# Kernel optimization log

Measured on AMD Instinct MI355X. Metric: run time of the kernel, lower is better.

Reference implementation:

```python
import jax, jax.numpy as jnp
import numpy as np

B, S = 4, 4096          # batch, tokens (64x64 SAM ViT-H grid)
DIN, DOUT = 1280, 3840  # qkv linear dims
RANK = 16
NUM_SHARED = 1
NUM_ROUTED = 6
TOP_K = 3


def setup_inputs() -> dict:
    key = jax.random.key(0)
    ks = jax.random.split(key, 9)
    s = 0.02
    return {
        "x": jax.random.normal(ks[0], (B, S, DIN), dtype=jnp.float32),
        "base_w": jax.random.normal(ks[1], (DIN, DOUT), dtype=jnp.float32) * s,
        "base_b": jax.random.normal(ks[2], (DOUT,), dtype=jnp.float32) * s,
        "shared_w1": jax.random.normal(ks[3], (NUM_SHARED, DIN, RANK), dtype=jnp.float32) * s,
        "shared_w2": jax.random.normal(ks[4], (NUM_SHARED, RANK, DOUT), dtype=jnp.float32) * s,
        "routed_w1": jax.random.normal(ks[5], (NUM_ROUTED, DIN, RANK), dtype=jnp.float32) * s,
        "routed_w2": jax.random.normal(ks[6], (NUM_ROUTED, RANK, DOUT), dtype=jnp.float32) * s,
        "router_w": jax.random.normal(ks[7], (DIN, NUM_ROUTED), dtype=jnp.float32) * s,
        "router_b": jax.random.normal(ks[8], (NUM_ROUTED,), dtype=jnp.float32) * s,
    }


def reference(x, base_w, base_b, shared_w1, shared_w2, routed_w1, routed_w2, router_w, router_b):
    b, s, din = x.shape
    # base linear runs under torch.no_grad() -> stop_gradient
    base = jax.lax.stop_gradient(jnp.einsum('bsi,io->bso', x, base_w) + base_b)
    # shared low-rank experts, summed over the shared set
    shared = jnp.einsum('bsi,eir,ero->bso', x, shared_w1, shared_w2)
    # router: softmax gates, top-k selection
    gates = jax.nn.softmax(x @ router_w + router_b, axis=-1)      # [B,S,E]
    topk_w, topk_idx = jax.lax.top_k(gates, TOP_K)                # [B,S,K]
    T = b * s
    xf = x.reshape(T, din)
    # combine weights: per-token weight for each expert (top-k indices are
    # distinct, so scatter-add reproduces the per-slot assignment exactly)
    cw = jnp.zeros((T, NUM_ROUTED), dtype=x.dtype).at[
        jnp.arange(T)[:, None], topk_idx.reshape(T, TOP_K)
    ].add(topk_w.reshape(T, TOP_K))                               # [T,E]
    # routed experts: contract rank and expert dims without materializing [T,E,DOUT]
    h = jnp.einsum('ti,eir->ter', xf, routed_w1)                  # [T,E,RANK]
    routed = jnp.einsum('ter,ero,te->to', h, routed_w2, cw).reshape(b, s, DOUT)
    return base + shared + routed
```

## Files before the change

kernel.cpp:

```cpp
#include <hip/hip_runtime.h>
#include <cstdint>
#include <cstddef>

#define DIN 1280
#define DOUT 3840
#define NEXP 6
#define RANK 16
#define TOKENS 16384
#define KPAD 1408
#define NLOW 128

typedef __bf16 bf16x8 __attribute__((ext_vector_type(8)));
typedef float f32x4 __attribute__((ext_vector_type(4)));
typedef unsigned short u16x8 __attribute__((ext_vector_type(8)));

__device__ __forceinline__ unsigned short f2bf(float f) {
    unsigned u = __builtin_bit_cast(unsigned, f);
    u += 0x7fff + ((u >> 16) & 1);
    return (unsigned short)(u >> 16);
}

__device__ __forceinline__ void async_load16(void* lds, const void* g) {
    __builtin_amdgcn_global_load_lds(
        (const __attribute__((address_space(1))) unsigned int*)g,
        (__attribute__((address_space(3))) unsigned int*)lds, 16, 0, 0);
}

__global__ void prep_w2t(const float* __restrict__ base_w,
                         const float* __restrict__ shared_w2,
                         const float* __restrict__ routed_w2,
                         unsigned short* __restrict__ WT) {
    __shared__ unsigned short tile[32][33];
    int k0 = blockIdx.x * 32, n0 = blockIdx.y * 32;
    int tx = threadIdx.x, ty = threadIdx.y;
#pragma unroll
    for (int j = 0; j < 4; j++) {
        int k = k0 + ty + j * 8;
        int n = n0 + tx;
        float v;
        if (k < DIN)            v = base_w[(size_t)k * DOUT + n];
        else if (k < DIN + 16)  v = shared_w2[(size_t)(k - DIN) * DOUT + n];
        else if (k < DIN + 112) v = routed_w2[(size_t)(k - DIN - 16) * DOUT + n];
        else                    v = 0.f;
        tile[ty + j * 8][tx] = f2bf(v);
    }
    __syncthreads();
#pragma unroll
    for (int j = 0; j < 4; j++) {
        int n = n0 + ty + j * 8;
        int k = k0 + tx;
        WT[(size_t)n * KPAD + k] = tile[tx][ty + j * 8];
    }
}

__global__ void prep_w1t(const float* __restrict__ shared_w1,
                         const float* __restrict__ routed_w1,
                         unsigned short* __restrict__ W1T) {
    __shared__ unsigned short tile[32][33];
    int k0 = blockIdx.x * 32, n0 = blockIdx.y * 32;
    int tx = threadIdx.x, ty = threadIdx.y;
#pragma unroll
    for (int j = 0; j < 4; j++) {
        int k = k0 + ty + j * 8;
        int n = n0 + tx;
        float v = 0.f;
        if (n < 16) v = shared_w1[k * RANK + n];
        else if (n < 112) {
            int jj = n - 16, e = jj >> 4, r = jj & 15;
            v = routed_w1[(size_t)e * DIN * RANK + k * RANK + r];
        }
        tile[ty + j * 8][tx] = f2bf(v);
    }
    __syncthreads();
#pragma unroll
    for (int j = 0; j < 4; j++) {
        int n = n0 + ty + j * 8;
        int k = k0 + tx;
        W1T[(size_t)n * DIN + k] = tile[tx][ty + j * 8];
    }
}

__global__ __launch_bounds__(256) void router_kernel(
    const float* __restrict__ x,
    const float* __restrict__ router_w,
    const float* __restrict__ router_b,
    unsigned short* __restrict__ A,
    float* __restrict__ cw) {
    int tid = threadIdx.x;
    size_t t0 = (size_t)blockIdx.x * 8;
    const float* xblk = x + t0 * DIN;
    unsigned short* Ablk = A + t0 * KPAD;

    for (int i = tid; i < 8 * (DIN / 8); i += 256) {
        int t = i / (DIN / 8), c = (i - t * (DIN / 8)) * 8;
        const float* xs = xblk + (size_t)t * DIN + c;
        f32x4 v0 = *(const f32x4*)xs;
        f32x4 v1 = *(const f32x4*)(xs + 4);
        u16x8 o;
#pragma unroll
        for (int j = 0; j < 4; j++) { o[j] = f2bf(v0[j]); o[4 + j] = f2bf(v1[j]); }
        *(u16x8*)&Ablk[(size_t)t * KPAD + c] = o;
    }
    if (tid < 128) {
        int t = tid >> 4, c = tid & 15;
        Ablk[t * KPAD + DIN + 112 + c] = 0;
    }

    int tg = tid >> 5, lj = tid & 31;
    const float* xt = xblk + (size_t)tg * DIN;
    float acc[6] = {0.f, 0.f, 0.f, 0.f, 0.f, 0.f};
    for (int k = lj; k < DIN; k += 32) {
        float xv = xt[k];
        const float* wr = router_w + k * NEXP;
#pragma unroll
        for (int e = 0; e < NEXP; e++) acc[e] = fmaf(xv, wr[e], acc[e]);
    }
#pragma unroll
    for (int off = 16; off > 0; off >>= 1)
#pragma unroll
        for (int e = 0; e < NEXP; e++) acc[e] += __shfl_xor(acc[e], off);

    float mx = -1e30f;
#pragma unroll
    for (int e = 0; e < NEXP; e++) { acc[e] += router_b[e]; mx = fmaxf(mx, acc[e]); }
    float g[6]; float s = 0.f;
#pragma unroll
    for (int e = 0; e < NEXP; e++) { g[e] = __expf(acc[e] - mx); s += g[e]; }
    float inv = 1.f / s;
    if (lj < NEXP) {
        float ge = g[lj];
        int cnt = 0;
#pragma unroll
        for (int e = 0; e < NEXP; e++) {
            if (e == lj) continue;
            if (g[e] > ge || (g[e] == ge && e < lj)) cnt++;
        }
        cw[(t0 + tg) * NEXP + lj] = (cnt < 3) ? ge * inv : 0.f;
    }
}

__global__ __launch_bounds__(256) void combine_kernel(
    const float* __restrict__ H, const float* __restrict__ cw,
    unsigned short* __restrict__ A) {
    int i = blockIdx.x * 256 + threadIdx.x;
    int t = i / 112, j = i - t * 112;
    float h = H[(size_t)t * NLOW + j] + H[(size_t)TOKENS * NLOW + (size_t)t * NLOW + j];
    float f = (j < 16) ? 1.0f : cw[t * NEXP + ((j - 16) >> 4)];
    A[(size_t)t * KPAD + DIN + j] = f2bf(f * h);
}

__global__ __launch_bounds__(256, 2) void gemm_small(
    const unsigned short* __restrict__ A,
    const unsigned short* __restrict__ BT,
    float* __restrict__ H) {
    __shared__ unsigned short ldsA[128 * 32];
    __shared__ unsigned short ldsB[128 * 32];
    const int KS = DIN / 2;
    int tid = threadIdx.x;
    int lane = tid & 63, wave = tid >> 6;
    int m0 = blockIdx.y * 128;
    int z = blockIdx.z;
    int wm = (wave >> 1) * 64, wn = (wave & 1) * 64;
    int lr = lane & 15, quad = lane >> 4;

    f32x4 acc[4][4] = {};
    const unsigned short* Abase = A + (size_t)m0 * KPAD + z * KS;
    const unsigned short* Bbase = BT + z * KS;
    float* Cbase = H + (size_t)z * TOKENS * NLOW;

    for (int k0 = 0; k0 < KS; k0 += 32) {
#pragma unroll
        for (int i = 0; i < 2; i++) {
            int c = i * 256 + tid;
            int row = c >> 2;
            int col = (c & 3) << 3;
            async_load16(&ldsA[(i * 256 + wave * 64) * 8],
                         Abase + (size_t)row * KPAD + k0 + col);
            async_load16(&ldsB[(i * 256 + wave * 64) * 8],
                         Bbase + (size_t)row * DIN + k0 + col);
        }
        __syncthreads();
        bf16x8 af[4], bf[4];
#pragma unroll
        for (int mi = 0; mi < 4; mi++)
            af[mi] = *(const bf16x8*)&ldsA[(wm + mi * 16 + lr) * 32 + quad * 8];
#pragma unroll
        for (int ni = 0; ni < 4; ni++)
            bf[ni] = *(const bf16x8*)&ldsB[(wn + ni * 16 + lr) * 32 + quad * 8];
#pragma unroll
        for (int mi = 0; mi < 4; mi++)
#pragma unroll
            for (int ni = 0; ni < 4; ni++)
                acc[mi][ni] = __builtin_amdgcn_mfma_f32_16x16x32_bf16(
                    af[mi], bf[ni], acc[mi][ni], 0, 0, 0);
        __syncthreads();
    }
#pragma unroll
    for (int ni = 0; ni < 4; ni++) {
        int gn = wn + ni * 16 + lr;
#pragma unroll
        for (int mi = 0; mi < 4; mi++) {
            int gm = m0 + wm + mi * 16 + quad * 4;
            f32x4 v = acc[mi][ni];
#pragma unroll
            for (int r = 0; r < 4; r++)
                Cbase[(size_t)(gm + r) * NLOW + gn] = v[r];
        }
    }
}


#define BM 256
#define BN 128
#define BKS 32

__global__ __launch_bounds__(512, 4) void gemm256(
    const unsigned short* __restrict__ A,
    const unsigned short* __restrict__ BT,
    const float* __restrict__ bias,
    float* __restrict__ C) {
    __shared__ unsigned short lA[2][BM * BKS];
    __shared__ unsigned short lB[2][BN * BKS];

    int tid = threadIdx.x;
    int lane = tid & 63, wave = tid >> 6;
    int bid = blockIdx.x;
    int xcd = bid & 7, lid = bid >> 3;
    int mt = xcd * 8 + (lid & 7);
    int nt = lid >> 3;
    int m0 = mt * BM, n0 = nt * BN;

    int wm = (wave >> 1) * 64, wn = (wave & 1) * 64;
    int lr = lane & 15, quad = lane >> 4;

    int srow = tid >> 2;
    int scg = (tid & 3) ^ ((tid >> 3) & 3);
    const unsigned short* aSrc = A + (size_t)(m0 + srow) * KPAD + scg * 8;
    const unsigned short* bSrc = BT + (size_t)(n0 + srow) * KPAD + scg * 8;

    f32x4 acc[4][4] = {};

    const int nkt = KPAD / BKS;
    {
        async_load16(&lA[0][0] + (size_t)tid * 8, aSrc);
        async_load16(&lA[0][0] + 128 * BKS + (size_t)tid * 8, aSrc + (size_t)128 * KPAD);
        async_load16(&lB[0][0] + (size_t)tid * 8, bSrc);
    }

#pragma unroll 2
    for (int t = 0; t < nkt; ++t) {
        __syncthreads();
        if (t + 1 < nkt) {
            int k1 = (t + 1) * BKS;
            unsigned short* dA = &lA[(t + 1) & 1][0];
            unsigned short* dB = &lB[(t + 1) & 1][0];
            async_load16(dA + (size_t)tid * 8, aSrc + k1);
            async_load16(dA + 128 * BKS + (size_t)tid * 8, aSrc + (size_t)128 * KPAD + k1);
            async_load16(dB + (size_t)tid * 8, bSrc + k1);
        }
        const unsigned short* a_cur = &lA[t & 1][0];
        const unsigned short* b_cur = &lB[t & 1][0];
        bf16x8 af[4], bf[4];
#pragma unroll
        for (int mi = 0; mi < 4; mi++) {
            int row = wm + mi * 16 + lr;
            int off = row * 64 + (((quad ^ ((row >> 1) & 3))) << 4);
            af[mi] = *(const bf16x8*)((const char*)a_cur + off);
        }
#pragma unroll
        for (int ni = 0; ni < 4; ni++) {
            int row = wn + ni * 16 + lr;
            int off = row * 64 + (((quad ^ ((row >> 1) & 3))) << 4);
            bf[ni] = *(const bf16x8*)((const char*)b_cur + off);
        }
#pragma unroll
        for (int mi = 0; mi < 4; mi++)
#pragma unroll
            for (int ni = 0; ni < 4; ni++)
                acc[mi][ni] = __builtin_amdgcn_mfma_f32_16x16x32_bf16(
                    af[mi], bf[ni], acc[mi][ni], 0, 0, 0);
    }

#pragma unroll
    for (int mi = 0; mi < 4; mi++) {
        int gm = m0 + wm + mi * 16 + quad * 4;
#pragma unroll
        for (int ni = 0; ni < 4; ni++) {
            int gn = n0 + wn + ni * 16 + lr;
            float bv = bias[gn];
            f32x4 v = acc[mi][ni];
#pragma unroll
            for (int r = 0; r < 4; r++)
                C[(size_t)(gm + r) * DOUT + gn] = v[r] + bv;
        }
    }
}

extern "C" void kernel_launch(void* const* d_in, const int* in_sizes, int n_in,
                              void* d_out, int out_size, void* d_ws, size_t ws_size,
                              hipStream_t stream) {
    const float* x         = (const float*)d_in[0];
    const float* base_w    = (const float*)d_in[1];
    const float* base_b    = (const float*)d_in[2];
    const float* shared_w1 = (const float*)d_in[3];
    const float* shared_w2 = (const float*)d_in[4];
    const float* routed_w1 = (const float*)d_in[5];
    const float* routed_w2 = (const float*)d_in[6];
    const float* router_w  = (const float*)d_in[7];
    const float* router_b  = (const float*)d_in[8];
    float* out = (float*)d_out;

    char* ws = (char*)d_ws;
    size_t off = 0;
    unsigned short* A     = (unsigned short*)(ws + off); off += (size_t)TOKENS * KPAD * 2;
    unsigned short* WcatT = (unsigned short*)(ws + off); off += (size_t)DOUT * KPAD * 2;
    unsigned short* W1T   = (unsigned short*)(ws + off); off += (size_t)NLOW * DIN * 2;
    float* H              = (float*)(ws + off);          off += (size_t)2 * TOKENS * NLOW * 4;
    float* cw             = (float*)(ws + off);          off += (size_t)TOKENS * NEXP * 4;

    prep_w2t<<<dim3(KPAD / 32, DOUT / 32), dim3(32, 8), 0, stream>>>(
        base_w, shared_w2, routed_w2, WcatT);
    prep_w1t<<<dim3(DIN / 32, NLOW / 32), dim3(32, 8), 0, stream>>>(
        shared_w1, routed_w1, W1T);
    router_kernel<<<TOKENS / 8, 256, 0, stream>>>(x, router_w, router_b, A, cw);
    gemm_small<<<dim3(1, TOKENS / 128, 2), 256, 0, stream>>>(A, W1T, H);
    combine_kernel<<<(TOKENS * 112) / 256, 256, 0, stream>>>(H, cw, A);
    gemm256<<<(DOUT / BN) * (TOKENS / BM), 512, 0, stream>>>(
        A, WcatT, base_b, out);
}
```

Before: 305.8 us.

## Load A fragments directly from global into registers and deepen B LDS pipeline

The main GEMM no longer stages A in LDS. Each wave owns 32 rows and loads its A fragments straight from global memory into registers, prefetching one k-step ahead. B now goes through a 4-deep LDS ring with explicit vmcnt waits, raw barriers and sched barriers, and MFMA blocks run at raised priority. The goal is to cut LDS traffic and barrier stalls, at the cost of uncoalesced per-lane global reads for A, lower occupancy from launch_bounds 2, and fragile hand-counted vmcnt values.

```diff
diff --git a/kernel.cpp b/kernel.cpp
--- a/kernel.cpp
+++ b/kernel.cpp
@@ -13,6 +13,9 @@
 typedef __bf16 bf16x8 __attribute__((ext_vector_type(8)));
 typedef float f32x4 __attribute__((ext_vector_type(4)));
 typedef unsigned short u16x8 __attribute__((ext_vector_type(8)));
+
+#define SB() __builtin_amdgcn_sched_barrier(0)
+#define BAR() __builtin_amdgcn_s_barrier()
 
 __device__ __forceinline__ unsigned short f2bf(float f) {
     unsigned u = __builtin_bit_cast(unsigned, f);
@@ -213,14 +216,14 @@
 #define BM 256
 #define BN 128
 #define BKS 32
-
-__global__ __launch_bounds__(512, 4) void gemm256(
+#define NKT (KPAD / BKS)
+
+__global__ __launch_bounds__(512, 2) void gemm256(
     const unsigned short* __restrict__ A,
     const unsigned short* __restrict__ BT,
     const float* __restrict__ bias,
     float* __restrict__ C) {
-    __shared__ unsigned short lA[2][BM * BKS];
-    __shared__ unsigned short lB[2][BN * BKS];
+    __shared__ unsigned short lB[4][BN * BKS];
 
     int tid = threadIdx.x;
     int lane = tid & 63, wave = tid >> 6;
@@ -230,63 +233,108 @@
     int nt = lid >> 3;
     int m0 = mt * BM, n0 = nt * BN;
 
-    int wm = (wave >> 1) * 64, wn = (wave & 1) * 64;
     int lr = lane & 15, quad = lane >> 4;
 
     int srow = tid >> 2;
     int scg = (tid & 3) ^ ((tid >> 3) & 3);
-    const unsigned short* aSrc = A + (size_t)(m0 + srow) * KPAD + scg * 8;
     const unsigned short* bSrc = BT + (size_t)(n0 + srow) * KPAD + scg * 8;
 
-    f32x4 acc[4][4] = {};
-
-    const int nkt = KPAD / BKS;
+    const unsigned short* aRow = A + (size_t)(m0 + wave * 32 + lr) * KPAD + quad * 8;
+
+    f32x4 acc[2][8] = {};
+    bf16x8 af[2][2];
+
+    auto stB = [&](int t) {
+        async_load16(&lB[t & 3][0] + (size_t)tid * 8, bSrc + (size_t)t * BKS);
+    };
+
+    stB(0);
+    stB(1);
+    af[0][0] = *(const bf16x8*)aRow;
+    af[0][1] = *(const bf16x8*)(aRow + (size_t)16 * KPAD);
+    SB();
+
+#pragma unroll 2
+    for (int t = 0; t < NKT - 2; ++t) {
+        const unsigned short* aT = aRow + (size_t)(t + 1) * BKS;
+        af[(t + 1) & 1][0] = *(const bf16x8*)aT;
+        af[(t + 1) & 1][1] = *(const bf16x8*)(aT + (size_t)16 * KPAD);
+        stB(t + 2);
+        SB();
+        asm volatile("s_waitcnt vmcnt(6)" ::: "memory");
+        SB(); BAR(); SB();
+        const unsigned short* b_cur = &lB[t & 3][0];
+        bf16x8 bf[8];
+#pragma unroll
+        for (int ni = 0; ni < 8; ni++) {
+            int row = ni * 16 + lr;
+            int off = row * 64 + ((quad ^ ((row >> 1) & 3)) << 4);
+            bf[ni] = *(const bf16x8*)((const char*)b_cur + off);
+        }
+        __builtin_amdgcn_s_setprio(1);
+#pragma unroll
+        for (int mi = 0; mi < 2; mi++)
+#pragma unroll
+            for (int ni = 0; ni < 8; ni++)
+                acc[mi][ni] = __builtin_amdgcn_mfma_f32_16x16x32_bf16(
+                    af[t & 1][mi], bf[ni], acc[mi][ni], 0, 0, 0);
+        __builtin_amdgcn_s_setprio(0);
+        SB();
+    }
+
     {
-        async_load16(&lA[0][0] + (size_t)tid * 8, aSrc);
-        async_load16(&lA[0][0] + 128 * BKS + (size_t)tid * 8, aSrc + (size_t)128 * KPAD);
-        async_load16(&lB[0][0] + (size_t)tid * 8, bSrc);
-    }
-
-#pragma unroll 2
-    for (int t = 0; t < nkt; ++t) {
-        __syncthreads();
-        if (t + 1 < nkt) {
-            int k1 = (t + 1) * BKS;
-            unsigned short* dA = &lA[(t + 1) & 1][0];
-            unsigned short* dB = &lB[(t + 1) & 1][0];
-            async_load16(dA + (size_t)tid * 8, aSrc + k1);
-            async_load16(dA + 128 * BKS + (size_t)tid * 8, aSrc + (size_t)128 * KPAD + k1);
-            async_load16(dB + (size_t)tid * 8, bSrc + k1);
-        }
-        const unsigned short* a_cur = &lA[t & 1][0];
-        const unsigned short* b_cur = &lB[t & 1][0];
-        bf16x8 af[4], bf[4];
-#pragma unroll
-        for (int mi = 0; mi < 4; mi++) {
-            int row = wm + mi * 16 + lr;
-            int off = row * 64 + (((quad ^ ((row >> 1) & 3))) << 4);
-            af[mi] = *(const bf16x8*)((const char*)a_cur + off);
-        }
-#pragma unroll
-        for (int ni = 0; ni < 4; ni++) {
-            int row = wn + ni * 16 + lr;
-            int off = row * 64 + (((quad ^ ((row >> 1) & 3))) << 4);
+        const unsigned short* aT = aRow + (size_t)43 * BKS;
+        af[1][0] = *(const bf16x8*)aT;
+        af[1][1] = *(const bf16x8*)(aT + (size_t)16 * KPAD);
+        SB();
+        asm volatile("s_waitcnt vmcnt(5)" ::: "memory");
+        SB(); BAR(); SB();
+        const unsigned short* b_cur = &lB[42 & 3][0];
+        bf16x8 bf[8];
+#pragma unroll
+        for (int ni = 0; ni < 8; ni++) {
+            int row = ni * 16 + lr;
+            int off = row * 64 + ((quad ^ ((row >> 1) & 3)) << 4);
             bf[ni] = *(const bf16x8*)((const char*)b_cur + off);
         }
-#pragma unroll
-        for (int mi = 0; mi < 4; mi++)
-#pragma unroll
-            for (int ni = 0; ni < 4; ni++)
+        __builtin_amdgcn_s_setprio(1);
+#pragma unroll
+        for (int mi = 0; mi < 2; mi++)
+#pragma unroll
+            for (int ni = 0; ni < 8; ni++)
                 acc[mi][ni] = __builtin_amdgcn_mfma_f32_16x16x32_bf16(
-                    af[mi], bf[ni], acc[mi][ni], 0, 0, 0);
-    }
-
-#pragma unroll
-    for (int mi = 0; mi < 4; mi++) {
-        int gm = m0 + wm + mi * 16 + quad * 4;
-#pragma unroll
-        for (int ni = 0; ni < 4; ni++) {
-            int gn = n0 + wn + ni * 16 + lr;
+                    af[0][mi], bf[ni], acc[mi][ni], 0, 0, 0);
+        __builtin_amdgcn_s_setprio(0);
+        SB();
+    }
+    {
+        asm volatile("s_waitcnt vmcnt(2)" ::: "memory");
+        SB(); BAR(); SB();
+        const unsigned short* b_cur = &lB[43 & 3][0];
+        bf16x8 bf[8];
+#pragma unroll
+        for (int ni = 0; ni < 8; ni++) {
+            int row = ni * 16 + lr;
+            int off = row * 64 + ((quad ^ ((row >> 1) & 3)) << 4);
+            bf[ni] = *(const bf16x8*)((const char*)b_cur + off);
+        }
+        __builtin_amdgcn_s_setprio(1);
+#pragma unroll
+        for (int mi = 0; mi < 2; mi++)
+#pragma unroll
+            for (int ni = 0; ni < 8; ni++)
+                acc[mi][ni] = __builtin_amdgcn_mfma_f32_16x16x32_bf16(
+                    af[1][mi], bf[ni], acc[mi][ni], 0, 0, 0);
+        __builtin_amdgcn_s_setprio(0);
+        SB();
+    }
+
+#pragma unroll
+    for (int mi = 0; mi < 2; mi++) {
+        int gm = m0 + wave * 32 + mi * 16 + quad * 4;
+#pragma unroll
+        for (int ni = 0; ni < 8; ni++) {
+            int gn = n0 + ni * 16 + lr;
             float bv = bias[gn];
             f32x4 v = acc[mi][ni];
 #pragma unroll
@@ -325,6 +373,6 @@
     router_kernel<<<TOKENS / 8, 256, 0, stream>>>(x, router_w, router_b, A, cw);
     gemm_small<<<dim3(1, TOKENS / 128, 2), 256, 0, stream>>>(A, W1T, H);
     combine_kernel<<<(TOKENS * 112) / 256, 256, 0, stream>>>(H, cw, A);
-    gemm256<<<(DOUT / BN) * (TOKENS / BM), 512, 0, stream>>>(
+    gemm256<<<(TOKENS / BM) * (DOUT / BN), 512, 0, stream>>>(
         A, WcatT, base_b, out);
 }
```

New measurement: 348.5 us. +14.0%, slower.
